# Kernel optimization log

Measured on AMD Instinct MI355X. Metric: run time of the kernel, lower is better.

The kernel has to match this reference:

```python
import jax, jax.numpy as jnp
import numpy as np

N_NODES = 50000
N_EDGES = 600000
N_GRAPHS = 2048
EMB = 128
N_LAYERS = 3
ATOM_FEATS, ATOM_VOCAB = 9, 100
BOND_FEATS, BOND_VOCAB, BOND_DIM = 3, 8, 3


def setup_inputs() -> dict:
    key = jax.random.key(0)
    ks = jax.random.split(key, 10)
    x = jax.random.randint(ks[0], (N_NODES, ATOM_FEATS), 0, ATOM_VOCAB)
    edge_index = jax.random.randint(ks[1], (2, N_EDGES), 0, N_NODES)
    edge_attr = jax.random.randint(ks[2], (N_EDGES, BOND_FEATS), 0, BOND_VOCAB)
    batch = jnp.sort(jax.random.randint(ks[3], (N_NODES,), 0, N_GRAPHS))
    s = 1.0 / np.sqrt(EMB).astype(np.float32)
    atom_emb = jax.random.normal(ks[4], (ATOM_FEATS, ATOM_VOCAB, EMB), jnp.float32) * 0.1
    bond_emb = jax.random.normal(ks[5], (N_LAYERS, BOND_FEATS, BOND_VOCAB, BOND_DIM), jnp.float32) * 0.1
    W = jax.random.normal(ks[6], (N_LAYERS, BOND_DIM, EMB, EMB), jnp.float32) * s
    b = jnp.zeros((N_LAYERS, BOND_DIM, EMB), jnp.float32)
    fc1_w = jax.random.normal(ks[7], (EMB, EMB), jnp.float32) * s
    fc1_b = jnp.zeros((EMB,), jnp.float32)
    fc2_w = jax.random.normal(ks[8], (EMB, 1), jnp.float32) * s
    fc2_b = jnp.zeros((1,), jnp.float32)
    return dict(x=x, edge_index=edge_index, edge_attr=edge_attr, batch=batch,
                atom_emb=atom_emb, bond_emb=bond_emb, W=W, b=b,
                fc1_w=fc1_w, fc1_b=fc1_b, fc2_w=fc2_w, fc2_b=fc2_b)


def reference(x, edge_index, edge_attr, batch, atom_emb, bond_emb, W, b,
              fc1_w, fc1_b, fc2_w, fc2_b):
    src, dst = edge_index[0], edge_index[1]
    n = x.shape[0]
    # AtomEncoder: sum of per-column embedding lookups -> [N, EMB]
    h = atom_emb[0][x[:, 0]]
    for c in range(1, ATOM_FEATS):
        h = h + atom_emb[c][x[:, c]]
    for layer in range(N_LAYERS):
        # BondEncoder: [E, BOND_DIM] edge weights (one scalar channel per conv)
        ew = bond_emb[layer, 0][edge_attr[:, 0]]
        for c in range(1, BOND_FEATS):
            ew = ew + bond_emb[layer, c][edge_attr[:, c]]
        # Three parallel GCNConv(normalize=False): linear, gather src, edge-weight, scatter-add to dst
        msg = jnp.zeros((edge_index.shape[1], EMB), h.dtype)
        for k in range(BOND_DIM):
            xw = h @ W[layer, k]              # [N, EMB]
            msg = msg + ew[:, k:k + 1] * xw[src]   # [E, EMB]
        agg = jax.ops.segment_sum(msg, dst, num_segments=n)
        hn = agg + jnp.sum(b[layer], axis=0)  # sum of the three conv biases
        if layer < N_LAYERS - 1:
            hn = jax.nn.relu(hn)              # dropout is identity at eval
        h = hn + h                            # residual
    # global_mean_pool
    sums = jax.ops.segment_sum(h, batch, num_segments=N_GRAPHS)
    counts = jax.ops.segment_sum(jnp.ones((n,), h.dtype), batch, num_segments=N_GRAPHS)
    hg = sums / jnp.maximum(counts, 1.0)[:, None]
    return (hg @ fc1_w + fc1_b) @ fc2_w + fc2_b   # [N_GRAPHS, 1]
```

## Files before the change

kernel.cpp:

```cpp
#include <hip/hip_runtime.h>

#define N_NODES 50000
#define N_EDGES 600000
#define N_GRAPHS 2048
#define EMB 128
#define TDIM 384
#define TS_LD 392
#define HN (N_NODES * EMB)
#define SCAN_NB ((N_NODES + 255) / 256)

#define PRE_ATOM_NB 8334
#define PRE_HIST_NB 1563
#define PRE_WCONV_NB 384
#define PRE_GB_NB 131

typedef __attribute__((ext_vector_type(8))) short bf16x8;
typedef __attribute__((ext_vector_type(4))) float f32x4;
#define MFMA_BF16(a, b, c) __builtin_amdgcn_mfma_f32_16x16x32_bf16(a, b, c, 0, 0, 0)

#define AS1 __attribute__((address_space(1)))
#define AS3 __attribute__((address_space(3)))
__device__ inline void gl_lds16(const void* g, void* l) {
  __builtin_amdgcn_global_load_lds((const AS1 void*)g, (AS3 void*)l, 16, 0, 0);
}

__device__ inline unsigned short f2bf(float f) {
  unsigned int u = __float_as_uint(f);
  u += 0x7fffu + ((u >> 16) & 1u);
  return (unsigned short)(u >> 16);
}
__device__ inline float bf2f(unsigned short b) {
  return __uint_as_float(((unsigned int)b) << 16);
}
__device__ inline bf16x8 pack8(float4 lo, float4 hi) {
  bf16x8 r;
  r[0] = (short)f2bf(lo.x); r[1] = (short)f2bf(lo.y);
  r[2] = (short)f2bf(lo.z); r[3] = (short)f2bf(lo.w);
  r[4] = (short)f2bf(hi.x); r[5] = (short)f2bf(hi.y);
  r[6] = (short)f2bf(hi.z); r[7] = (short)f2bf(hi.w);
  return r;
}

__global__ __launch_bounds__(384) void k_pre(const int* __restrict__ x,
                                             const float* __restrict__ atom_emb,
                                             unsigned short* __restrict__ h_bf,
                                             const int* __restrict__ ei,
                                             int* __restrict__ deg,
                                             const float* __restrict__ W,
                                             unsigned short* __restrict__ wt,
                                             const int* __restrict__ batch,
                                             int* __restrict__ gs) {
  __shared__ float sb[6 * 1280];
  int blk = blockIdx.x;
  if (blk < PRE_ATOM_NB) {
    const int wv = threadIdx.x >> 6;
    const int lane = threadIdx.x & 63;
    int n = blk * 6 + wv;
    if (n < N_NODES) {
      const int nu = __builtin_amdgcn_readfirstlane(n);
      const int* xr = x + nu * 9;
      int ix[9];
#pragma unroll
      for (int c = 0; c < 9; ++c) ix[c] = xr[c];
      float* wbase = sb + wv * 1280;
      const int half = lane >> 5;
      const int sub16 = lane & 31;
#pragma unroll
      for (int j = 0; j < 4; ++j) {
        int c = 2 * j + half;
        const float* g = atom_emb + (size_t)(c * 100 + ix[c]) * EMB + sub16 * 4;
        gl_lds16(g, wbase + j * 256);
      }
      {
        const float* g = atom_emb + (size_t)(8 * 100 + ix[8]) * EMB + sub16 * 4;
        gl_lds16(g, wbase + 1024);
      }
      asm volatile("s_waitcnt vmcnt(0)" ::: "memory");
      float2 acc = {0.f, 0.f};
#pragma unroll
      for (int c = 0; c < 9; ++c) {
        float2 v = *(const float2*)(wbase + c * 128 + lane * 2);
        acc.x += v.x; acc.y += v.y;
      }
      *(ushort2*)(h_bf + (size_t)nu * EMB + lane * 2) = ushort2{f2bf(acc.x), f2bf(acc.y)};
    }
    return;
  }
  blk -= PRE_ATOM_NB;
  if (blk < PRE_HIST_NB) {
    int e = blk * 384 + threadIdx.x;
    if (e < N_EDGES) atomicAdd(&deg[ei[N_EDGES + e]], 1);
    return;
  }
  blk -= PRE_HIST_NB;
  if (blk < PRE_WCONV_NB) {
    int layer = blk >> 7, c = blk & 127, k = threadIdx.x;
    float v = W[(((layer * 3 + (k >> 7)) * 128) + (k & 127)) * 128 + c];
    wt[(size_t)blk * 384 + k] = f2bf(v);
    return;
  }
  blk -= PRE_WCONV_NB;
  {
    int i = blk * 384 + threadIdx.x;
    if (i < N_NODES) {
      int b = batch[i];
      int bp = (i == 0) ? -1 : batch[i - 1];
      for (int g = bp + 1; g <= b; ++g) gs[g] = i;
      if (i == N_NODES - 1) {
        for (int g = b + 1; g <= N_GRAPHS; ++g) gs[g] = N_NODES;
      }
    }
  }
}

__global__ __launch_bounds__(256) void k_scan_a(const int* __restrict__ deg,
                                                int* __restrict__ row_start,
                                                int* __restrict__ partials) {
  __shared__ int s[256];
  const int tid = threadIdx.x;
  const int i = blockIdx.x * 256 + tid;
  int v = (i < N_NODES) ? deg[i] : 0;
  s[tid] = v;
  __syncthreads();
  for (int off = 1; off < 256; off <<= 1) {
    int t = (tid >= off) ? s[tid - off] : 0;
    __syncthreads();
    s[tid] += t;
    __syncthreads();
  }
  if (i < N_NODES) row_start[i] = s[tid] - v;
  if (tid == 255) partials[blockIdx.x] = s[255];
}

__global__ __launch_bounds__(256) void k_scan_b(int* __restrict__ partials,
                                                int* __restrict__ row_start) {
  __shared__ int s[256];
  const int tid = threadIdx.x;
  int v = (tid < SCAN_NB) ? partials[tid] : 0;
  s[tid] = v;
  __syncthreads();
  for (int off = 1; off < 256; off <<= 1) {
    int t = (tid >= off) ? s[tid - off] : 0;
    __syncthreads();
    s[tid] += t;
    __syncthreads();
  }
  if (tid < SCAN_NB) partials[tid] = s[tid] - v;
  if (tid == 255) row_start[N_NODES] = s[255];
}

__global__ __launch_bounds__(256) void k_scan_c(int* __restrict__ row_start,
                                                const int* __restrict__ partials,
                                                int* __restrict__ cursor) {
  const int i = blockIdx.x * 256 + threadIdx.x;
  if (i < N_NODES) {
    int r = row_start[i] + partials[blockIdx.x];
    row_start[i] = r;
    cursor[i] = r;
  }
}

__global__ __launch_bounds__(256) void k_scatter(const int* __restrict__ ei,
                                                 const int* __restrict__ ea,
                                                 int* __restrict__ cursor,
                                                 int2* __restrict__ sorted_se) {
  int e = blockIdx.x * 256 + threadIdx.x;
  if (e >= N_EDGES) return;
  int src = ei[e], dst = ei[N_EDGES + e];
  int pos = atomicAdd(&cursor[dst], 1);
  int eap = ea[e * 3 + 0] | (ea[e * 3 + 1] << 3) | (ea[e * 3 + 2] << 6);
  sorted_se[pos] = int2{src, eap};
}

__global__ __launch_bounds__(256) void k_agg(const int2* __restrict__ sorted_se,
                                             const int* __restrict__ row_start,
                                             const float* __restrict__ bl,
                                             const unsigned short* __restrict__ h_bf,
                                             unsigned short* __restrict__ t_bf) {
  __shared__ float4 combo[512];
  for (int c = threadIdx.x; c < 512; c += 256) {
    int a0 = c & 7, a1 = (c >> 3) & 7, a2 = (c >> 6) & 7;
    combo[c] = float4{bl[a0 * 3 + 0] + bl[24 + a1 * 3 + 0] + bl[48 + a2 * 3 + 0],
                      bl[a0 * 3 + 1] + bl[24 + a1 * 3 + 1] + bl[48 + a2 * 3 + 1],
                      bl[a0 * 3 + 2] + bl[24 + a1 * 3 + 2] + bl[48 + a2 * 3 + 2], 0.f};
  }
  __syncthreads();
  const int node = blockIdx.x * 16 + (threadIdx.x >> 4);
  const int sub = threadIdx.x & 15;
  const int beg = row_start[node], end = row_start[node + 1];
  float4 l0 = {0.f, 0.f, 0.f, 0.f}, h0 = l0;
  float4 l1 = l0, h1 = l0;
  float4 l2 = l0, h2 = l0;
  int e = beg;
  const int full_end = beg + ((end - beg) & ~7);
  for (; e < full_end; e += 8) {
    int2 se[8];
#pragma unroll
    for (int j = 0; j < 8; ++j) se[j] = sorted_se[e + j];
    bf16x8 u[8];
#pragma unroll
    for (int j = 0; j < 8; ++j)
      u[j] = *(const bf16x8*)(h_bf + (size_t)se[j].x * EMB + sub * 8);
#pragma unroll
    for (int j = 0; j < 8; ++j) {
      float4 w = combo[se[j].y];
      float4 vlo = {bf2f((unsigned short)u[j][0]), bf2f((unsigned short)u[j][1]),
                    bf2f((unsigned short)u[j][2]), bf2f((unsigned short)u[j][3])};
      float4 vhi = {bf2f((unsigned short)u[j][4]), bf2f((unsigned short)u[j][5]),
                    bf2f((unsigned short)u[j][6]), bf2f((unsigned short)u[j][7])};
      l0 += vlo * w.x; h0 += vhi * w.x;
      l1 += vlo * w.y; h1 += vhi * w.y;
      l2 += vlo * w.z; h2 += vhi * w.z;
    }
  }
  if (e < end) {
    int2 se[8];
#pragma unroll
    for (int j = 0; j < 8; ++j) {
      int idx = e + j;
      se[j] = sorted_se[idx < end ? idx : end - 1];
    }
    bf16x8 u[8];
#pragma unroll
    for (int j = 0; j < 8; ++j)
      u[j] = *(const bf16x8*)(h_bf + (size_t)se[j].x * EMB + sub * 8);
#pragma unroll
    for (int j = 0; j < 8; ++j) {
      float4 w = (e + j < end) ? combo[se[j].y] : float4{0.f, 0.f, 0.f, 0.f};
      float4 vlo = {bf2f((unsigned short)u[j][0]), bf2f((unsigned short)u[j][1]),
                    bf2f((unsigned short)u[j][2]), bf2f((unsigned short)u[j][3])};
      float4 vhi = {bf2f((unsigned short)u[j][4]), bf2f((unsigned short)u[j][5]),
                    bf2f((unsigned short)u[j][6]), bf2f((unsigned short)u[j][7])};
      l0 += vlo * w.x; h0 += vhi * w.x;
      l1 += vlo * w.y; h1 += vhi * w.y;
      l2 += vlo * w.z; h2 += vhi * w.z;
    }
  }
  size_t base = (size_t)node * TDIM + sub * 8;
  *(bf16x8*)(t_bf + base)       = pack8(l0, h0);
  *(bf16x8*)(t_bf + base + 128) = pack8(l1, h1);
  *(bf16x8*)(t_bf + base + 256) = pack8(l2, h2);
}

__global__ __launch_bounds__(512) void k_gemm(const unsigned short* __restrict__ t_bf,
                                              const unsigned short* __restrict__ wt,
                                              const float* __restrict__ bl,
                                              const unsigned short* __restrict__ h_in_bf,
                                              unsigned short* __restrict__ h_out_bf,
                                              int do_relu) {
  __shared__ unsigned short ts[32 * TS_LD];
  const int nb = blockIdx.x * 32;
  for (int i = threadIdx.x; i < 32 * 48; i += 512) {
    int r = i / 48, cc = i % 48;
    bf16x8 v = {};
    int row = nb + r;
    if (row < N_NODES) v = *(const bf16x8*)(t_bf + (size_t)row * TDIM + cc * 8);
    *(bf16x8*)(ts + r * TS_LD + cc * 8) = v;
  }
  __syncthreads();

  const int wv = threadIdx.x >> 6;
  const int lane = threadIdx.x & 63;
  const int m = lane & 15;
  const int kq = lane >> 4;
  const int c = wv * 16 + m;

  const unsigned short* pB = wt + (size_t)c * TDIM + kq * 8;
  bf16x8 B[12];
#pragma unroll
  for (int kc = 0; kc < 12; ++kc) B[kc] = *(const bf16x8*)(pB + kc * 32);

  const float bias = bl[c] + bl[128 + c] + bl[256 + c];

#pragma unroll
  for (int rt = 0; rt < 2; ++rt) {
    const unsigned short* pA = ts + (rt * 16 + m) * TS_LD + kq * 8;
    bf16x8 A[12];
#pragma unroll
    for (int kc = 0; kc < 12; ++kc) A[kc] = *(const bf16x8*)(pA + kc * 32);
    f32x4 acc = {0.f, 0.f, 0.f, 0.f};
#pragma unroll
    for (int kc = 0; kc < 12; ++kc) acc = MFMA_BF16(A[kc], B[kc], acc);
#pragma unroll
    for (int r = 0; r < 4; ++r) {
      int row = nb + rt * 16 + kq * 4 + r;
      if (row < N_NODES) {
        size_t idx = (size_t)row * EMB + c;
        float v = acc[r] + bias;
        if (do_relu) v = fmaxf(v, 0.f);
        float hn = bf2f(h_in_bf[idx]) + v;
        h_out_bf[idx] = f2bf(hn);
      }
    }
  }
}

__global__ __launch_bounds__(128) void k_head(const unsigned short* __restrict__ h_bf,
                                              const int* __restrict__ gs,
                                              const float* __restrict__ fc1_w,
                                              const float* __restrict__ fc1_b,
                                              const float* __restrict__ fc2_w,
                                              const float* __restrict__ fc2_b,
                                              float* __restrict__ out) {
  __shared__ float hg[EMB];
  __shared__ float red[EMB];
  int g = blockIdx.x, e = threadIdx.x;
  int ns = gs[g], ne = gs[g + 1];
  float acc = 0.f;
  for (int n = ns; n < ne; ++n) acc += bf2f(h_bf[(size_t)n * EMB + e]);
  float cnt = fmaxf((float)(ne - ns), 1.f);
  hg[e] = acc / cnt;
  __syncthreads();
  float a2 = fc1_b[e];
  for (int j = 0; j < EMB; ++j) a2 += hg[j] * fc1_w[j * EMB + e];
  red[e] = a2 * fc2_w[e];
  __syncthreads();
  for (int s = 64; s > 0; s >>= 1) {
    if (e < s) red[e] += red[e + s];
    __syncthreads();
  }
  if (e == 0) out[g] = red[0] + fc2_b[0];
}

extern "C" void kernel_launch(void* const* d_in, const int* in_sizes, int n_in,
                              void* d_out, int out_size, void* d_ws, size_t ws_size,
                              hipStream_t stream) {
  const int*   x        = (const int*)d_in[0];
  const int*   ei       = (const int*)d_in[1];
  const int*   ea       = (const int*)d_in[2];
  const int*   batch    = (const int*)d_in[3];
  const float* atom_emb = (const float*)d_in[4];
  const float* bond_emb = (const float*)d_in[5];
  const float* W        = (const float*)d_in[6];
  const float* b        = (const float*)d_in[7];
  const float* fc1_w    = (const float*)d_in[8];
  const float* fc1_b    = (const float*)d_in[9];
  const float* fc2_w    = (const float*)d_in[10];
  const float* fc2_b    = (const float*)d_in[11];
  float* out = (float*)d_out;

  char* p = (char*)d_ws;
  auto alloc = [&](size_t bytes) { char* r = p; p += (bytes + 255) & ~(size_t)255; return r; };
  unsigned short* h0_bf      = (unsigned short*)alloc((size_t)HN * 2);
  unsigned short* h1_bf      = (unsigned short*)alloc((size_t)HN * 2);
  unsigned short* t_bf       = (unsigned short*)alloc((size_t)N_NODES * TDIM * 2);
  unsigned short* wt         = (unsigned short*)alloc((size_t)3 * 128 * TDIM * 2);
  int*            gs         = (int*)alloc((size_t)(N_GRAPHS + 1) * 4);
  int*            deg        = (int*)alloc((size_t)N_NODES * 4);
  int*            row_start  = (int*)alloc((size_t)(N_NODES + 1) * 4);
  int*            cursor     = (int*)alloc((size_t)N_NODES * 4);
  int*            partials   = (int*)alloc(256 * 4);
  int2*           sorted_se  = (int2*)alloc((size_t)(N_EDGES + 8) * 8);

  hipMemsetAsync(deg, 0, N_NODES * sizeof(int), stream);
  const int pre_blocks = PRE_ATOM_NB + PRE_HIST_NB + PRE_WCONV_NB + PRE_GB_NB;
  k_pre<<<pre_blocks, 384, 0, stream>>>(x, atom_emb, h0_bf, ei, deg, W, wt, batch, gs);
  k_scan_a<<<SCAN_NB, 256, 0, stream>>>(deg, row_start, partials);
  k_scan_b<<<1, 256, 0, stream>>>(partials, row_start);
  k_scan_c<<<SCAN_NB, 256, 0, stream>>>(row_start, partials, cursor);
  k_scatter<<<(N_EDGES + 255) / 256, 256, 0, stream>>>(ei, ea, cursor, sorted_se);

  unsigned short* hib = h0_bf;
  unsigned short* hob = h1_bf;
  const int gemm_blocks = (N_NODES + 31) / 32;
  for (int layer = 0; layer < 3; ++layer) {
    k_agg<<<N_NODES / 16, 256, 0, stream>>>(sorted_se, row_start, bond_emb + layer * 72,
                                            hib, t_bf);
    k_gemm<<<gemm_blocks, 512, 0, stream>>>(
        t_bf, wt + (size_t)layer * 128 * TDIM, b + layer * 3 * EMB,
        hib, hob, layer < 2 ? 1 : 0);
    unsigned short* tb = hib; hib = hob; hob = tb;
  }

  k_head<<<N_GRAPHS, 128, 0, stream>>>(hib, gs, fc1_w, fc1_b, fc2_w, fc2_b, out);
}
```

Measured before the change: 360.8 us.

## Replace scatter-phase atomics with precomputed ranks from a 4-way replicated histogram

```diff
diff --git a/kernel.cpp b/kernel.cpp
--- a/kernel.cpp
+++ b/kernel.cpp
@@ -45,7 +45,8 @@
                                              const float* __restrict__ atom_emb,
                                              unsigned short* __restrict__ h_bf,
                                              const int* __restrict__ ei,
-                                             int* __restrict__ deg,
+                                             int* __restrict__ deg4,
+                                             int* __restrict__ rank,
                                              const float* __restrict__ W,
                                              unsigned short* __restrict__ wt,
                                              const int* __restrict__ batch,
@@ -89,7 +90,11 @@
   blk -= PRE_ATOM_NB;
   if (blk < PRE_HIST_NB) {
     int e = blk * 384 + threadIdx.x;
-    if (e < N_EDGES) atomicAdd(&deg[ei[N_EDGES + e]], 1);
+    if (e < N_EDGES) {
+      int d = ei[N_EDGES + e];
+      int r = blk & 3;
+      rank[e] = atomicAdd(&deg4[r * N_NODES + d], 1);
+    }
     return;
   }
   blk -= PRE_HIST_NB;
@@ -113,13 +118,22 @@
   }
 }
 
-__global__ __launch_bounds__(256) void k_scan_a(const int* __restrict__ deg,
+__global__ __launch_bounds__(256) void k_scan_a(const int* __restrict__ deg4,
                                                 int* __restrict__ row_start,
-                                                int* __restrict__ partials) {
+                                                int* __restrict__ partials,
+                                                int* __restrict__ base4) {
   __shared__ int s[256];
   const int tid = threadIdx.x;
   const int i = blockIdx.x * 256 + tid;
-  int v = (i < N_NODES) ? deg[i] : 0;
+  int v = 0;
+  if (i < N_NODES) {
+    int d0 = deg4[i];
+    int d1 = deg4[N_NODES + i];
+    int d2 = deg4[2 * N_NODES + i];
+    int d3 = deg4[3 * N_NODES + i];
+    v = d0 + d1 + d2 + d3;
+    base4[i] = (d0 << 8) | ((d0 + d1) << 16) | ((unsigned)(d0 + d1 + d2) << 24);
+  }
   s[tid] = v;
   __syncthreads();
   for (int off = 1; off < 256; off <<= 1) {
@@ -150,24 +164,23 @@
 }
 
 __global__ __launch_bounds__(256) void k_scan_c(int* __restrict__ row_start,
-                                                const int* __restrict__ partials,
-                                                int* __restrict__ cursor) {
+                                                const int* __restrict__ partials) {
   const int i = blockIdx.x * 256 + threadIdx.x;
-  if (i < N_NODES) {
-    int r = row_start[i] + partials[blockIdx.x];
-    row_start[i] = r;
-    cursor[i] = r;
-  }
+  if (i < N_NODES) row_start[i] += partials[blockIdx.x];
 }
 
 __global__ __launch_bounds__(256) void k_scatter(const int* __restrict__ ei,
                                                  const int* __restrict__ ea,
-                                                 int* __restrict__ cursor,
+                                                 const int* __restrict__ rank,
+                                                 const int* __restrict__ row_start,
+                                                 const int* __restrict__ base4,
                                                  int2* __restrict__ sorted_se) {
   int e = blockIdx.x * 256 + threadIdx.x;
   if (e >= N_EDGES) return;
   int src = ei[e], dst = ei[N_EDGES + e];
-  int pos = atomicAdd(&cursor[dst], 1);
+  int r = (e / 384) & 3;
+  int base = (base4[dst] >> (r * 8)) & 255;
+  int pos = row_start[dst] + base + rank[e];
   int eap = ea[e * 3 + 0] | (ea[e * 3 + 1] << 3) | (ea[e * 3 + 2] << 6);
   sorted_se[pos] = int2{src, eap};
 }
@@ -346,19 +359,20 @@
   unsigned short* t_bf       = (unsigned short*)alloc((size_t)N_NODES * TDIM * 2);
   unsigned short* wt         = (unsigned short*)alloc((size_t)3 * 128 * TDIM * 2);
   int*            gs         = (int*)alloc((size_t)(N_GRAPHS + 1) * 4);
-  int*            deg        = (int*)alloc((size_t)N_NODES * 4);
+  int*            deg4       = (int*)alloc((size_t)4 * N_NODES * 4);
+  int*            rank       = (int*)alloc((size_t)N_EDGES * 4);
+  int*            base4      = (int*)alloc((size_t)N_NODES * 4);
   int*            row_start  = (int*)alloc((size_t)(N_NODES + 1) * 4);
-  int*            cursor     = (int*)alloc((size_t)N_NODES * 4);
   int*            partials   = (int*)alloc(256 * 4);
   int2*           sorted_se  = (int2*)alloc((size_t)(N_EDGES + 8) * 8);
 
-  hipMemsetAsync(deg, 0, N_NODES * sizeof(int), stream);
+  hipMemsetAsync(deg4, 0, 4 * N_NODES * sizeof(int), stream);
   const int pre_blocks = PRE_ATOM_NB + PRE_HIST_NB + PRE_WCONV_NB + PRE_GB_NB;
-  k_pre<<<pre_blocks, 384, 0, stream>>>(x, atom_emb, h0_bf, ei, deg, W, wt, batch, gs);
-  k_scan_a<<<SCAN_NB, 256, 0, stream>>>(deg, row_start, partials);
+  k_pre<<<pre_blocks, 384, 0, stream>>>(x, atom_emb, h0_bf, ei, deg4, rank, W, wt, batch, gs);
+  k_scan_a<<<SCAN_NB, 256, 0, stream>>>(deg4, row_start, partials, base4);
   k_scan_b<<<1, 256, 0, stream>>>(partials, row_start);
-  k_scan_c<<<SCAN_NB, 256, 0, stream>>>(row_start, partials, cursor);
-  k_scatter<<<(N_EDGES + 255) / 256, 256, 0, stream>>>(ei, ea, cursor, sorted_se);
+  k_scan_c<<<SCAN_NB, 256, 0, stream>>>(row_start, partials);
+  k_scatter<<<(N_EDGES + 255) / 256, 256, 0, stream>>>(ei, ea, rank, row_start, base4, sorted_se);
 
   unsigned short* hib = h0_bf;
   unsigned short* hob = h1_bf;
```

New measurement: 348.3 us. 3.5% less time.
